# Optimization experiments

Measured on AMD Instinct MI355X. Metric: run time of the kernel, lower is better.

## Reference

```python
import jax, jax.numpy as jnp
import numpy as np

B, S, H = 32, 1024, 512  # S = DIM*DIM with DIM=32

def setup_inputs() -> dict:
    key = jax.random.key(0)
    ks = jax.random.split(key, 8)
    sd = 1.0 / np.sqrt(H)
    return {
        "x": jax.random.normal(ks[0], (B, S, H), jnp.float32),
        "mask": jax.random.uniform(ks[1], (B, S, S), jnp.float32),
        "Wq": jax.random.normal(ks[2], (H, H), jnp.float32) * sd,
        "bq": jnp.zeros((H,), jnp.float32),
        "Wk": jax.random.normal(ks[3], (H, H), jnp.float32) * sd,
        "bk": jnp.zeros((H,), jnp.float32),
        "Wv": jax.random.normal(ks[4], (H, H), jnp.float32) * sd,
        "bv": jnp.zeros((H,), jnp.float32),
    }

def reference(x, mask, Wq, bq, Wk, bk, Wv, bv):
    # Linear projections (torch Linear: x @ W^T + b)
    Q = jnp.einsum('bsh,oh->bso', x, Wq) + bq
    K = jnp.einsum('bsh,oh->bso', x, Wk) + bk
    V = jnp.einsum('bsh,oh->bso', x, Wv) + bv
    scale = jnp.sqrt(jnp.asarray(Q.shape[-1], Q.dtype))
    energy = jnp.einsum('bqh,bkh->bqk', Q, K) / scale  # [B,S,S]
    attention = jax.nn.softmax(energy, axis=-1)
    A = attention * mask
    # Original computes global sum of A per batch via two matmuls with ones vectors;
    # equivalent to a full reduction over both S dims -> [B,1,1]
    denom = jnp.sum(A, axis=(1, 2), keepdims=True)
    ma = jnp.einsum('bqk,bkh->bqh', A, V) / denom
    return ma
```

## Files before the change

kernel.cpp:

```cpp
#include <hip/hip_runtime.h>
#include <stdint.h>

#define NB 32
#define SL 1024
#define HD 512
#define NS (NB * SL)

typedef __attribute__((ext_vector_type(8))) short short8;
typedef __attribute__((ext_vector_type(4))) short short4v;
typedef __attribute__((ext_vector_type(4))) float f32x4;

__device__ __forceinline__ unsigned short f2bf(float f) {
    union { float f; uint32_t u; } c; c.f = f;
    uint32_t u = c.u;
    return (unsigned short)((u + 0x7FFFu + ((u >> 16) & 1u)) >> 16);
}

__device__ __forceinline__ void gl_lds16(const void* g, void* l) {
    __builtin_amdgcn_global_load_lds(
        (const __attribute__((address_space(1))) uint32_t*)g,
        (__attribute__((address_space(3))) uint32_t*)l, 16, 0, 0);
}

__device__ __forceinline__ f32x4 ntload4(const float* p) {
    return __builtin_nontemporal_load((const f32x4*)p);
}

__global__ void k_cvt(const float* __restrict__ in, unsigned short* __restrict__ out, int n8) {
    int i = blockIdx.x * blockDim.x + threadIdx.x;
    int stride = gridDim.x * blockDim.x;
    for (; i < n8; i += stride) {
        const float4* p = (const float4*)in + (size_t)i * 2;
        float4 a = p[0], b = p[1];
        short8 v;
        v[0] = (short)f2bf(a.x); v[1] = (short)f2bf(a.y);
        v[2] = (short)f2bf(a.z); v[3] = (short)f2bf(a.w);
        v[4] = (short)f2bf(b.x); v[5] = (short)f2bf(b.y);
        v[6] = (short)f2bf(b.z); v[7] = (short)f2bf(b.w);
        *((short8*)out + i) = v;
    }
}

__global__ void k_cvtw(const float* __restrict__ Wq, const float* __restrict__ Wk,
                       const float* __restrict__ Wv,
                       unsigned short* __restrict__ Wqk, unsigned short* __restrict__ Wvb,
                       float* __restrict__ den) {
    const int C8 = HD * HD / 8;
    int i = blockIdx.x * blockDim.x + threadIdx.x;
    const float* src; unsigned short* dst; int j;
    if (i < C8)            { src = Wq; dst = Wqk;            j = i; }
    else if (i < 2 * C8)   { src = Wk; dst = Wqk + HD * HD;  j = i - C8; }
    else if (i < 3 * C8)   { src = Wv; dst = Wvb;            j = i - 2 * C8; }
    else return;
    const float4* p = (const float4*)src + (size_t)j * 2;
    float4 a = p[0], b = p[1];
    short8 v;
    v[0] = (short)f2bf(a.x); v[1] = (short)f2bf(a.y);
    v[2] = (short)f2bf(a.z); v[3] = (short)f2bf(a.w);
    v[4] = (short)f2bf(b.x); v[5] = (short)f2bf(b.y);
    v[6] = (short)f2bf(b.z); v[7] = (short)f2bf(b.w);
    *((short8*)dst + j) = v;
    if (i < NB) den[i] = 0.f;
}

template<int BIAS_M>
__global__ __launch_bounds__(256, 4)
void k_gemm_bt(const unsigned short* __restrict__ A,
               const unsigned short* __restrict__ Bm,
               const float* __restrict__ bias,
               const float* __restrict__ bias2,
               int nsplit,
               unsigned short* __restrict__ C,
               int M, int N, int K) {
    __shared__ unsigned short As[128 * 64];
    __shared__ unsigned short Bs[128 * 64];
    const int t = threadIdx.x;
    const int lane = t & 63, w = t >> 6;
    const int wr = w >> 1, wc = w & 1;
    const int g = lane >> 4, lr = lane & 15;
    const int m0 = blockIdx.y * 128, n0 = blockIdx.x * 128;

    f32x4 acc[4][4];
#pragma unroll
    for (int i = 0; i < 4; i++)
#pragma unroll
        for (int j = 0; j < 4; j++) acc[i][j] = (f32x4){0.f, 0.f, 0.f, 0.f};

    for (int kt = 0; kt < K; kt += 64) {
#pragma unroll
        for (int i = 0; i < 4; i++) {
            int u = i * 256 + t;
            int row = u >> 3, c = u & 7;
            int sc = c ^ (row & 7);
            gl_lds16(A + (size_t)(m0 + row) * K + kt + sc * 8,
                     (char*)As + (size_t)(i * 256 + w * 64) * 16);
        }
#pragma unroll
        for (int i = 0; i < 4; i++) {
            int u = i * 256 + t;
            int row = u >> 3, c = u & 7;
            int sc = c ^ (row & 7);
            gl_lds16(Bm + (size_t)(n0 + row) * K + kt + sc * 8,
                     (char*)Bs + (size_t)(i * 256 + w * 64) * 16);
        }
        __syncthreads();
#pragma unroll
        for (int ks = 0; ks < 2; ks++) {
            short8 af[4], bf[4];
#pragma unroll
            for (int mf = 0; mf < 4; mf++) {
                int row = wr * 64 + mf * 16 + lr;
                int ch = (ks * 4 + g) ^ (row & 7);
                af[mf] = *(const short8*)((const char*)As + row * 128 + ch * 16);
            }
#pragma unroll
            for (int nf = 0; nf < 4; nf++) {
                int row = wc * 64 + nf * 16 + lr;
                int ch = (ks * 4 + g) ^ (row & 7);
                bf[nf] = *(const short8*)((const char*)Bs + row * 128 + ch * 16);
            }
#pragma unroll
            for (int mf = 0; mf < 4; mf++)
#pragma unroll
                for (int nf = 0; nf < 4; nf++)
                    acc[mf][nf] = __builtin_amdgcn_mfma_f32_16x16x32_bf16(
                        af[mf], bf[nf], acc[mf][nf], 0, 0, 0);
        }
        __syncthreads();
    }
#pragma unroll
    for (int mf = 0; mf < 4; mf++) {
#pragma unroll
        for (int nf = 0; nf < 4; nf++) {
            int col = n0 + wc * 64 + nf * 16 + lr;
            int row0 = m0 + wr * 64 + mf * 16 + g * 4;
            float cb = 0.f;
            if (!BIAS_M) cb = (col < nsplit) ? bias[col] : bias2[col - nsplit];
#pragma unroll
            for (int r = 0; r < 4; r++) {
                float v = acc[mf][nf][r] + (BIAS_M ? bias[row0 + r] : cb);
                C[(size_t)(row0 + r) * N + col] = f2bf(v);
            }
        }
    }
}

__global__ __launch_bounds__(1024, 4)
void k_flash(const unsigned short* __restrict__ QK,
             const unsigned short* __restrict__ Vt,
             const float* __restrict__ mask,
             float* __restrict__ out,
             float* __restrict__ denom) {
    __shared__ unsigned short Qs[64 * 512];
    __shared__ unsigned short Ps[64 * 512];
    __shared__ float wredL[16 * 64];
    __shared__ float wredA[16 * 64];
    __shared__ float tredL[64];
    __shared__ float tredA[64];

    const int t = threadIdx.x;
    const int lane = t & 63, w = t >> 6;
    const int g = lane >> 4, lr = lane & 15;
    const int bid = blockIdx.x;
    const int nid = (bid & 7) * 64 + (bid >> 3);
    const int b = nid >> 4, qt = nid & 15;
    const int q0 = qt * 64;

    const unsigned short* Qg = QK + (size_t)(b * SL + q0) * 1024;
#pragma unroll
    for (int i = 0; i < 4; i++) {
        int u = i * 1024 + t;
        int row = u >> 6, c = u & 63;
        int sc = c ^ (row & 7);
        gl_lds16(Qg + (size_t)row * 1024 + sc * 8,
                 (char*)Qs + (size_t)(i * 1024 + w * 64) * 16);
    }

    f32x4 O[4][2];
    float lsum[4], asum[4];
#pragma unroll
    for (int qf = 0; qf < 4; qf++) {
        lsum[qf] = 0.f; asum[qf] = 0.f;
        O[qf][0] = (f32x4){0.f, 0.f, 0.f, 0.f};
        O[qf][1] = (f32x4){0.f, 0.f, 0.f, 0.f};
    }
    __syncthreads();

    const float iscale = 0.04419417382415922f;

    for (int kt = 0; kt < 2; kt++) {
        f32x4 P[2][4];
#pragma unroll
        for (int kf = 0; kf < 2; kf++)
#pragma unroll
            for (int qf = 0; qf < 4; qf++) P[kf][qf] = (f32x4){0.f, 0.f, 0.f, 0.f};

        const unsigned short* Kg = QK + 512 + (size_t)(b * SL + kt * 512 + w * 32) * 1024;
#pragma unroll 4
        for (int h = 0; h < HD; h += 32) {
            short8 ka[2], qb[4];
#pragma unroll
            for (int kf = 0; kf < 2; kf++)
                ka[kf] = *(const short8*)(Kg + (size_t)(kf * 16 + lr) * 1024 + h + g * 8);
#pragma unroll
            for (int qf = 0; qf < 4; qf++) {
                int q = qf * 16 + lr;
                int sc = ((h >> 3) + g) ^ (q & 7);
                qb[qf] = *(const short8*)((const char*)Qs + q * 1024 + sc * 16);
            }
#pragma unroll
            for (int kf = 0; kf < 2; kf++)
#pragma unroll
                for (int qf = 0; qf < 4; qf++)
                    P[kf][qf] = __builtin_amdgcn_mfma_f32_16x16x32_bf16(
                        ka[kf], qb[qf], P[kf][qf], 0, 0, 0);
        }

        if (kt) __syncthreads();

        const float* mrow = mask + ((size_t)(b * SL + q0)) * SL + kt * 512 + w * 32;
        f32x4 mv[4][2];
#pragma unroll
        for (int qf = 0; qf < 4; qf++)
#pragma unroll
            for (int kf = 0; kf < 2; kf++)
                mv[qf][kf] = ntload4(mrow + (size_t)(qf * 16 + lr) * SL + kf * 16 + g * 4);

#pragma unroll
        for (int qf = 0; qf < 4; qf++) {
            int q = qf * 16 + lr;
#pragma unroll
            for (int kf = 0; kf < 2; kf++) {
                f32x4 e;
#pragma unroll
                for (int r = 0; r < 4; r++) e[r] = __expf(P[kf][qf][r] * iscale);
                lsum[qf] += e[0] + e[1] + e[2] + e[3];
                f32x4 a = e * mv[qf][kf];
                asum[qf] += a[0] + a[1] + a[2] + a[3];
                short4v pk;
                pk[0] = (short)f2bf(a[0]); pk[1] = (short)f2bf(a[1]);
                pk[2] = (short)f2bf(a[2]); pk[3] = (short)f2bf(a[3]);
                int chunk = w * 4 + kf * 2 + (g >> 1);
                int sc = chunk ^ (q & 7);
                *(short4v*)((char*)Ps + q * 1024 + sc * 16 + (g & 1) * 8) = pk;
            }
        }
        __syncthreads();

        const unsigned short* Vg = Vt + (size_t)(w * 32) * NS + (size_t)b * SL + kt * 512;
#pragma unroll 4
        for (int ks = 0; ks < 512; ks += 32) {
            short8 pa[4], vb[2];
#pragma unroll
            for (int qf = 0; qf < 4; qf++) {
                int q = qf * 16 + lr;
                int sc = ((ks >> 3) + g) ^ (q & 7);
                pa[qf] = *(const short8*)((const char*)Ps + q * 1024 + sc * 16);
            }
#pragma unroll
            for (int nh = 0; nh < 2; nh++)
                vb[nh] = *(const short8*)(Vg + (size_t)(nh * 16 + lr) * NS + ks + g * 8);
#pragma unroll
            for (int qf = 0; qf < 4; qf++)
#pragma unroll
                for (int nh = 0; nh < 2; nh++)
                    O[qf][nh] = __builtin_amdgcn_mfma_f32_16x16x32_bf16(
                        pa[qf], vb[nh], O[qf][nh], 0, 0, 0);
        }
    }

#pragma unroll
    for (int qf = 0; qf < 4; qf++) {
        float L = lsum[qf], A = asum[qf];
        L += __shfl_xor(L, 16); L += __shfl_xor(L, 32);
        A += __shfl_xor(A, 16); A += __shfl_xor(A, 32);
        if (g == 0) {
            wredL[w * 64 + qf * 16 + lr] = L;
            wredA[w * 64 + qf * 16 + lr] = A;
        }
    }
    __syncthreads();
    if (t < 64) {
        float L = 0.f, A = 0.f;
#pragma unroll
        for (int ww = 0; ww < 16; ww++) { L += wredL[ww * 64 + t]; A += wredA[ww * 64 + t]; }
        tredL[t] = L; tredA[t] = A;
    }
    __syncthreads();

#pragma unroll
    for (int qf = 0; qf < 4; qf++) {
        f32x4 Lv = *(const f32x4*)&tredL[qf * 16 + g * 4];
#pragma unroll
        for (int r = 0; r < 4; r++) {
            float invl = 1.0f / Lv[r];
            size_t rowoff = (size_t)(b * SL + q0 + qf * 16 + g * 4 + r) * HD;
#pragma unroll
            for (int nh = 0; nh < 2; nh++)
                out[rowoff + w * 32 + nh * 16 + lr] = O[qf][nh][r] * invl;
        }
    }
    if (t < 64) {
        float d = tredA[t] / tredL[t];
        d += __shfl_xor(d, 1); d += __shfl_xor(d, 2); d += __shfl_xor(d, 4);
        d += __shfl_xor(d, 8); d += __shfl_xor(d, 16); d += __shfl_xor(d, 32);
        if (lane == 0) atomicAdd(&denom[b], d);
    }
}

__global__ void k_norm(float* __restrict__ out, const float* __restrict__ denom) {
    const int n4 = NB * SL * HD / 4;
    int i = blockIdx.x * blockDim.x + threadIdx.x;
    int stride = gridDim.x * blockDim.x;
    for (; i < n4; i += stride) {
        int b = i >> 17;
        float inv = 1.0f / denom[b];
        float4 v = ((float4*)out)[i];
        v.x *= inv; v.y *= inv; v.z *= inv; v.w *= inv;
        ((float4*)out)[i] = v;
    }
}

extern "C" void kernel_launch(void* const* d_in, const int* in_sizes, int n_in,
                              void* d_out, int out_size, void* d_ws, size_t ws_size,
                              hipStream_t stream) {
    const float* x    = (const float*)d_in[0];
    const float* mask = (const float*)d_in[1];
    const float* Wq   = (const float*)d_in[2];
    const float* bq   = (const float*)d_in[3];
    const float* Wk   = (const float*)d_in[4];
    const float* bk   = (const float*)d_in[5];
    const float* Wv   = (const float*)d_in[6];
    const float* bv   = (const float*)d_in[7];
    float* out = (float*)d_out;

    const size_t SZ_X = (size_t)NS * HD * 2;
    const size_t SZ_W = (size_t)HD * HD * 2;

    size_t off = 0;
    char* base = (char*)d_ws;
    unsigned short* xb  = (unsigned short*)(base + off); off += SZ_X;
    unsigned short* Vt  = (unsigned short*)(base + off); off += SZ_X;
    unsigned short* QKm = (unsigned short*)(base + off); off += 2 * SZ_X;
    unsigned short* Wqk = (unsigned short*)(base + off); off += 2 * SZ_W;
    unsigned short* Wvb = (unsigned short*)(base + off); off += SZ_W;
    float* den = (float*)(base + off); off += 256;

    hipLaunchKernelGGL(k_cvt, dim3(2048), dim3(256), 0, stream, x, xb, NS * HD / 8);
    hipLaunchKernelGGL(k_cvtw, dim3(384), dim3(256), 0, stream, Wq, Wk, Wv, Wqk, Wvb, den);

    hipLaunchKernelGGL((k_gemm_bt<0>), dim3(1024 / 128, NS / 128), dim3(256), 0, stream,
                       xb, Wqk, bq, bk, HD, QKm, NS, 1024, HD);
    hipLaunchKernelGGL((k_gemm_bt<1>), dim3(NS / 128, HD / 128), dim3(256), 0, stream,
                       Wvb, xb, bv, bv, 1 << 30, Vt, HD, NS, HD);

    hipLaunchKernelGGL(k_flash, dim3(512), dim3(1024), 0, stream,
                       QKm, Vt, mask, out, den);
    hipLaunchKernelGGL(k_norm, dim3(2048), dim3(256), 0, stream, out, den);
}
```

Before: 528.6 us.

## Merge conversion and projection launches, halve flash query tile, remap norm blocks

Fuses the x and weight bf16 conversions into one launch and both projection GEMMs into a single grid with XCD-aware block swizzles. The flash kernel now uses 32-row query tiles with 1024 blocks and a higher occupancy bound, and issues mask loads before the QK MFMA loop to hide their latency. The normalization kernel assigns one tile per block with the same swizzle so it can hit data still cached from the flash pass. Smaller query tiles mean K and V are re-read from memory twice as often, which costs extra bandwidth.

```diff
diff --git a/kernel.cpp b/kernel.cpp
--- a/kernel.cpp
+++ b/kernel.cpp
@@ -26,32 +26,7 @@
     return __builtin_nontemporal_load((const f32x4*)p);
 }
 
-__global__ void k_cvt(const float* __restrict__ in, unsigned short* __restrict__ out, int n8) {
-    int i = blockIdx.x * blockDim.x + threadIdx.x;
-    int stride = gridDim.x * blockDim.x;
-    for (; i < n8; i += stride) {
-        const float4* p = (const float4*)in + (size_t)i * 2;
-        float4 a = p[0], b = p[1];
-        short8 v;
-        v[0] = (short)f2bf(a.x); v[1] = (short)f2bf(a.y);
-        v[2] = (short)f2bf(a.z); v[3] = (short)f2bf(a.w);
-        v[4] = (short)f2bf(b.x); v[5] = (short)f2bf(b.y);
-        v[6] = (short)f2bf(b.z); v[7] = (short)f2bf(b.w);
-        *((short8*)out + i) = v;
-    }
-}
-
-__global__ void k_cvtw(const float* __restrict__ Wq, const float* __restrict__ Wk,
-                       const float* __restrict__ Wv,
-                       unsigned short* __restrict__ Wqk, unsigned short* __restrict__ Wvb,
-                       float* __restrict__ den) {
-    const int C8 = HD * HD / 8;
-    int i = blockIdx.x * blockDim.x + threadIdx.x;
-    const float* src; unsigned short* dst; int j;
-    if (i < C8)            { src = Wq; dst = Wqk;            j = i; }
-    else if (i < 2 * C8)   { src = Wk; dst = Wqk + HD * HD;  j = i - C8; }
-    else if (i < 3 * C8)   { src = Wv; dst = Wvb;            j = i - 2 * C8; }
-    else return;
+__device__ __forceinline__ void cvt8(const float* src, unsigned short* dst, int j) {
     const float4* p = (const float4*)src + (size_t)j * 2;
     float4 a = p[0], b = p[1];
     short8 v;
@@ -60,25 +35,42 @@
     v[4] = (short)f2bf(b.x); v[5] = (short)f2bf(b.y);
     v[6] = (short)f2bf(b.z); v[7] = (short)f2bf(b.w);
     *((short8*)dst + j) = v;
+}
+
+__global__ void k_cvtall(const float* __restrict__ x,
+                         const float* __restrict__ Wq, const float* __restrict__ Wk,
+                         const float* __restrict__ Wv,
+                         unsigned short* __restrict__ xb,
+                         unsigned short* __restrict__ Wqk, unsigned short* __restrict__ Wvb,
+                         float* __restrict__ den) {
+    const int XC = NS * HD / 8;
+    const int WC = HD * HD / 8;
+    int i = blockIdx.x * blockDim.x + threadIdx.x;
+    if (i < XC) {
+        cvt8(x, xb, i);
+    } else {
+        int j = i - XC;
+        if (j < WC)            cvt8(Wq, Wqk, j);
+        else if (j < 2 * WC)   cvt8(Wk, Wqk + HD * HD, j - WC);
+        else                   cvt8(Wv, Wvb, j - 2 * WC);
+    }
     if (i < NB) den[i] = 0.f;
 }
 
 template<int BIAS_M>
-__global__ __launch_bounds__(256, 4)
-void k_gemm_bt(const unsigned short* __restrict__ A,
+__device__ __forceinline__
+void gemm_tile(const unsigned short* __restrict__ A,
                const unsigned short* __restrict__ Bm,
                const float* __restrict__ bias,
                const float* __restrict__ bias2,
                int nsplit,
                unsigned short* __restrict__ C,
-               int M, int N, int K) {
-    __shared__ unsigned short As[128 * 64];
-    __shared__ unsigned short Bs[128 * 64];
+               int m0, int n0, int N, int K,
+               unsigned short* As, unsigned short* Bs) {
     const int t = threadIdx.x;
     const int lane = t & 63, w = t >> 6;
     const int wr = w >> 1, wc = w & 1;
     const int g = lane >> 4, lr = lane & 15;
-    const int m0 = blockIdx.y * 128, n0 = blockIdx.x * 128;
 
     f32x4 acc[4][4];
 #pragma unroll
@@ -145,30 +137,55 @@
     }
 }
 
-__global__ __launch_bounds__(1024, 4)
+__global__ __launch_bounds__(256, 4)
+void k_gemm2(const unsigned short* __restrict__ xb,
+             const unsigned short* __restrict__ Wqk,
+             const unsigned short* __restrict__ Wvb,
+             const float* __restrict__ bq, const float* __restrict__ bk,
+             const float* __restrict__ bv,
+             unsigned short* __restrict__ QKm,
+             unsigned short* __restrict__ Vt) {
+    __shared__ unsigned short As[128 * 64];
+    __shared__ unsigned short Bs[128 * 64];
+    int bid = blockIdx.x;
+    if (bid < 2048) {
+        int nid = (bid & 7) * 256 + (bid >> 3);
+        int bx = nid & 7, by = nid >> 3;
+        gemm_tile<0>(xb, Wqk, bq, bk, HD, QKm,
+                     by * 128, bx * 128, 1024, HD, As, Bs);
+    } else {
+        int b2 = bid - 2048;
+        int nid = (b2 & 7) * 128 + (b2 >> 3);
+        int x = nid >> 2, y = nid & 3;
+        gemm_tile<1>(Wvb, xb, bv, bv, 1 << 30, Vt,
+                     y * 128, x * 128, NS, HD, As, Bs);
+    }
+}
+
+__global__ __launch_bounds__(1024, 8)
 void k_flash(const unsigned short* __restrict__ QK,
              const unsigned short* __restrict__ Vt,
              const float* __restrict__ mask,
              float* __restrict__ out,
              float* __restrict__ denom) {
-    __shared__ unsigned short Qs[64 * 512];
-    __shared__ unsigned short Ps[64 * 512];
-    __shared__ float wredL[16 * 64];
-    __shared__ float wredA[16 * 64];
-    __shared__ float tredL[64];
-    __shared__ float tredA[64];
+    __shared__ unsigned short Qs[32 * 512];
+    __shared__ unsigned short Ps[32 * 512];
+    __shared__ float wredL[16 * 32];
+    __shared__ float wredA[16 * 32];
+    __shared__ float tredL[32];
+    __shared__ float tredA[32];
 
     const int t = threadIdx.x;
     const int lane = t & 63, w = t >> 6;
     const int g = lane >> 4, lr = lane & 15;
     const int bid = blockIdx.x;
-    const int nid = (bid & 7) * 64 + (bid >> 3);
-    const int b = nid >> 4, qt = nid & 15;
-    const int q0 = qt * 64;
+    const int nid = (bid & 7) * 128 + (bid >> 3);
+    const int b = nid >> 5, qt = nid & 31;
+    const int q0 = qt * 32;
 
     const unsigned short* Qg = QK + (size_t)(b * SL + q0) * 1024;
 #pragma unroll
-    for (int i = 0; i < 4; i++) {
+    for (int i = 0; i < 2; i++) {
         int u = i * 1024 + t;
         int row = u >> 6, c = u & 63;
         int sc = c ^ (row & 7);
@@ -176,10 +193,10 @@
                  (char*)Qs + (size_t)(i * 1024 + w * 64) * 16);
     }
 
-    f32x4 O[4][2];
-    float lsum[4], asum[4];
-#pragma unroll
-    for (int qf = 0; qf < 4; qf++) {
+    f32x4 O[2][2];
+    float lsum[2], asum[2];
+#pragma unroll
+    for (int qf = 0; qf < 2; qf++) {
         lsum[qf] = 0.f; asum[qf] = 0.f;
         O[qf][0] = (f32x4){0.f, 0.f, 0.f, 0.f};
         O[qf][1] = (f32x4){0.f, 0.f, 0.f, 0.f};
@@ -189,21 +206,29 @@
     const float iscale = 0.04419417382415922f;
 
     for (int kt = 0; kt < 2; kt++) {
-        f32x4 P[2][4];
+        const float* mrow = mask + ((size_t)(b * SL + q0)) * SL + kt * 512 + w * 32;
+        f32x4 mv[2][2];
+#pragma unroll
+        for (int qf = 0; qf < 2; qf++)
+#pragma unroll
+            for (int kf = 0; kf < 2; kf++)
+                mv[qf][kf] = ntload4(mrow + (size_t)(qf * 16 + lr) * SL + kf * 16 + g * 4);
+
+        f32x4 P[2][2];
 #pragma unroll
         for (int kf = 0; kf < 2; kf++)
 #pragma unroll
-            for (int qf = 0; qf < 4; qf++) P[kf][qf] = (f32x4){0.f, 0.f, 0.f, 0.f};
+            for (int qf = 0; qf < 2; qf++) P[kf][qf] = (f32x4){0.f, 0.f, 0.f, 0.f};
 
         const unsigned short* Kg = QK + 512 + (size_t)(b * SL + kt * 512 + w * 32) * 1024;
 #pragma unroll 4
         for (int h = 0; h < HD; h += 32) {
-            short8 ka[2], qb[4];
+            short8 ka[2], qb[2];
 #pragma unroll
             for (int kf = 0; kf < 2; kf++)
                 ka[kf] = *(const short8*)(Kg + (size_t)(kf * 16 + lr) * 1024 + h + g * 8);
 #pragma unroll
-            for (int qf = 0; qf < 4; qf++) {
+            for (int qf = 0; qf < 2; qf++) {
                 int q = qf * 16 + lr;
                 int sc = ((h >> 3) + g) ^ (q & 7);
                 qb[qf] = *(const short8*)((const char*)Qs + q * 1024 + sc * 16);
@@ -211,23 +236,15 @@
 #pragma unroll
             for (int kf = 0; kf < 2; kf++)
 #pragma unroll
-                for (int qf = 0; qf < 4; qf++)
+                for (int qf = 0; qf < 2; qf++)
                     P[kf][qf] = __builtin_amdgcn_mfma_f32_16x16x32_bf16(
                         ka[kf], qb[qf], P[kf][qf], 0, 0, 0);
         }
 
         if (kt) __syncthreads();
 
-        const float* mrow = mask + ((size_t)(b * SL + q0)) * SL + kt * 512 + w * 32;
-        f32x4 mv[4][2];
-#pragma unroll
-        for (int qf = 0; qf < 4; qf++)
-#pragma unroll
-            for (int kf = 0; kf < 2; kf++)
-                mv[qf][kf] = ntload4(mrow + (size_t)(qf * 16 + lr) * SL + kf * 16 + g * 4);
-
-#pragma unroll
-        for (int qf = 0; qf < 4; qf++) {
+#pragma unroll
+        for (int qf = 0; qf < 2; qf++) {
             int q = qf * 16 + lr;
 #pragma unroll
             for (int kf = 0; kf < 2; kf++) {
@@ -250,9 +267,9 @@
         const unsigned short* Vg = Vt + (size_t)(w * 32) * NS + (size_t)b * SL + kt * 512;
 #pragma unroll 4
         for (int ks = 0; ks < 512; ks += 32) {
-            short8 pa[4], vb[2];
-#pragma unroll
-            for (int qf = 0; qf < 4; qf++) {
+            short8 pa[2], vb[2];
+#pragma unroll
+            for (int qf = 0; qf < 2; qf++) {
                 int q = qf * 16 + lr;
                 int sc = ((ks >> 3) + g) ^ (q & 7);
                 pa[qf] = *(const short8*)((const char*)Ps + q * 1024 + sc * 16);
@@ -261,7 +278,7 @@
             for (int nh = 0; nh < 2; nh++)
                 vb[nh] = *(const short8*)(Vg + (size_t)(nh * 16 + lr) * NS + ks + g * 8);
 #pragma unroll
-            for (int qf = 0; qf < 4; qf++)
+            for (int qf = 0; qf < 2; qf++)
 #pragma unroll
                 for (int nh = 0; nh < 2; nh++)
                     O[qf][nh] = __builtin_amdgcn_mfma_f32_16x16x32_bf16(
@@ -270,26 +287,26 @@
     }
 
 #pragma unroll
-    for (int qf = 0; qf < 4; qf++) {
+    for (int qf = 0; qf < 2; qf++) {
         float L = lsum[qf], A = asum[qf];
         L += __shfl_xor(L, 16); L += __shfl_xor(L, 32);
         A += __shfl_xor(A, 16); A += __shfl_xor(A, 32);
         if (g == 0) {
-            wredL[w * 64 + qf * 16 + lr] = L;
-            wredA[w * 64 + qf * 16 + lr] = A;
+            wredL[w * 32 + qf * 16 + lr] = L;
+            wredA[w * 32 + qf * 16 + lr] = A;
         }
     }
     __syncthreads();
-    if (t < 64) {
+    if (t < 32) {
         float L = 0.f, A = 0.f;
 #pragma unroll
-        for (int ww = 0; ww < 16; ww++) { L += wredL[ww * 64 + t]; A += wredA[ww * 64 + t]; }
+        for (int ww = 0; ww < 16; ww++) { L += wredL[ww * 32 + t]; A += wredA[ww * 32 + t]; }
         tredL[t] = L; tredA[t] = A;
     }
     __syncthreads();
 
 #pragma unroll
-    for (int qf = 0; qf < 4; qf++) {
+    for (int qf = 0; qf < 2; qf++) {
         f32x4 Lv = *(const f32x4*)&tredL[qf * 16 + g * 4];
 #pragma unroll
         for (int r = 0; r < 4; r++) {
@@ -300,24 +317,25 @@
                 out[rowoff + w * 32 + nh * 16 + lr] = O[qf][nh][r] * invl;
         }
     }
-    if (t < 64) {
+    if (t < 32) {
         float d = tredA[t] / tredL[t];
         d += __shfl_xor(d, 1); d += __shfl_xor(d, 2); d += __shfl_xor(d, 4);
-        d += __shfl_xor(d, 8); d += __shfl_xor(d, 16); d += __shfl_xor(d, 32);
-        if (lane == 0) atomicAdd(&denom[b], d);
+        d += __shfl_xor(d, 8); d += __shfl_xor(d, 16);
+        if (t == 0) atomicAdd(&denom[b], d);
     }
 }
 
 __global__ void k_norm(float* __restrict__ out, const float* __restrict__ denom) {
-    const int n4 = NB * SL * HD / 4;
-    int i = blockIdx.x * blockDim.x + threadIdx.x;
-    int stride = gridDim.x * blockDim.x;
-    for (; i < n4; i += stride) {
-        int b = i >> 17;
-        float inv = 1.0f / denom[b];
-        float4 v = ((float4*)out)[i];
+    const int bid = blockIdx.x;
+    const int nid = (bid & 7) * 128 + (bid >> 3);
+    const int b = nid >> 5;
+    const float inv = 1.0f / denom[b];
+    float4* p = (float4*)out + (size_t)nid * 4096;
+#pragma unroll 4
+    for (int j = threadIdx.x; j < 4096; j += 256) {
+        float4 v = p[j];
         v.x *= inv; v.y *= inv; v.z *= inv; v.w *= inv;
-        ((float4*)out)[i] = v;
+        p[j] = v;
     }
 }
 
@@ -346,15 +364,13 @@
     unsigned short* Wvb = (unsigned short*)(base + off); off += SZ_W;
     float* den = (float*)(base + off); off += 256;
 
-    hipLaunchKernelGGL(k_cvt, dim3(2048), dim3(256), 0, stream, x, xb, NS * HD / 8);
-    hipLaunchKernelGGL(k_cvtw, dim3(384), dim3(256), 0, stream, Wq, Wk, Wv, Wqk, Wvb, den);
-
-    hipLaunchKernelGGL((k_gemm_bt<0>), dim3(1024 / 128, NS / 128), dim3(256), 0, stream,
-                       xb, Wqk, bq, bk, HD, QKm, NS, 1024, HD);
-    hipLaunchKernelGGL((k_gemm_bt<1>), dim3(NS / 128, HD / 128), dim3(256), 0, stream,
-                       Wvb, xb, bv, bv, 1 << 30, Vt, HD, NS, HD);
-
-    hipLaunchKernelGGL(k_flash, dim3(512), dim3(1024), 0, stream,
+    hipLaunchKernelGGL(k_cvtall, dim3(8576), dim3(256), 0, stream,
+                       x, Wq, Wk, Wv, xb, Wqk, Wvb, den);
+
+    hipLaunchKernelGGL(k_gemm2, dim3(3072), dim3(256), 0, stream,
+                       xb, Wqk, Wvb, bq, bk, bv, QKm, Vt);
+
+    hipLaunchKernelGGL(k_flash, dim3(1024), dim3(1024), 0, stream,
                        QKm, Vt, mask, out, den);
-    hipLaunchKernelGGL(k_norm, dim3(2048), dim3(256), 0, stream, out, den);
-}
+    hipLaunchKernelGGL(k_norm, dim3(1024), dim3(256), 0, stream, out, den);
+}
```

After: 706.2 us. +33.6%, slower.
